# Kernel optimization log

Hardware: AMD Instinct MI355X
Metric: run time of the kernel (lower is better)

The kernel has to match this reference:

```python
import jax, jax.numpy as jnp
import numpy as np

V, D, H, B, S, K = 10000, 128, 512, 32, 512, 2  # vocab, emb, hidden, batch, seq, num_cells

def setup_inputs() -> dict:
    key = jax.random.key(0)
    ks = jax.random.split(key, 8)
    sc_d, sc_h = 1.0 / np.sqrt(D), 1.0 / np.sqrt(H)
    return {
        "x": jax.random.randint(ks[0], (B, S), 0, V),
        "emb_table": jax.random.normal(ks[1], (V, D), jnp.float32),
        "W_ih": jax.random.uniform(ks[2], (K, 4 * H, D), jnp.float32, -sc_d, sc_d),
        "W_hh": jax.random.uniform(ks[3], (K, 4 * H, H), jnp.float32, -sc_h, sc_h),
        "b_ih": jax.random.uniform(ks[4], (K, 4 * H), jnp.float32, -sc_h, sc_h),
        "b_hh": jax.random.uniform(ks[5], (K, 4 * H), jnp.float32, -sc_h, sc_h),
        "W_out": jax.random.uniform(ks[6], (V, H), jnp.float32, -sc_h, sc_h),
        "b_out": jax.random.uniform(ks[7], (V,), jnp.float32, -sc_h, sc_h),
    }

def _mlstm(x_ids_t, emb_t, W_ih, W_hh, b, h0, c0):
    # x_ids_t: (S,B) int, emb_t: (S,B,D). Two LSTMCells; token id parity picks the cell.
    def step(carry, inp):
        h, c = carry                       # (B,H) each
        xt, ids = inp                      # (B,D), (B,)
        gates = (jnp.einsum('bd,kgd->kbg', xt, W_ih)
                 + jnp.einsum('bh,kgh->kbg', h, W_hh)
                 + b[:, None, :])          # (K,B,4H)
        i, f, g, o = jnp.split(gates, 4, axis=-1)
        i, f, o = jax.nn.sigmoid(i), jax.nn.sigmoid(f), jax.nn.sigmoid(o)
        g = jnp.tanh(g)
        c_new = f * c + i * g              # (K,B,H)
        h_new = o * jnp.tanh(c_new)        # (K,B,H)
        sel = (ids % 2)[:, None]           # (B,1) cell index per example
        h_next = jnp.where(sel == 0, h_new[0], h_new[1])
        c_next = jnp.where(sel == 0, c_new[0], c_new[1])
        return (h_next, c_next), h_next
    (_, _), hs = jax.lax.scan(step, (h0, c0), (emb_t, x_ids_t))
    return hs  # (S,B,H)

def reference(x, emb_table, W_ih, W_hh, b_ih, b_hh, W_out, b_out):
    emb = emb_table[x]                     # (B,S,D)
    emb_t = jnp.transpose(emb, (1, 0, 2))  # (S,B,D) time-major
    h0 = jnp.zeros((x.shape[0], W_hh.shape[-1]), emb.dtype)
    hs = _mlstm(x.T, emb_t, W_ih, W_hh, b_ih + b_hh, h0, h0)  # (S,B,H)
    flat = hs.reshape(-1, hs.shape[-1])    # (S*B, H)
    logits = flat @ W_out.T + b_out        # (S*B, V)
    return jax.nn.log_softmax(logits, axis=1)
```

## Files before the change

### kernel.cpp

```cpp
#include <hip/hip_runtime.h>
#include <hip/hip_bf16.h>

typedef __attribute__((ext_vector_type(8))) short short8;
typedef __attribute__((ext_vector_type(4))) float f32x4;
typedef unsigned long long u64;

#define V_N 10000
#define D_E 128
#define H_N 512
#define B_N 32
#define S_N 512

#define SENT64 0xFFFFFFFFFFFFFFFFull

#define OFF_RP    0
#define OFF_EMB   5242880
#define OFF_HS    (OFF_EMB + 4194304)
#define OFF_WOUT  (OFF_HS + 16777216)

__device__ __forceinline__ float ftanh(float x) {
  float e = __expf(-2.f * fabsf(x));
  float r = (1.f - e) / (1.f + e);
  return __builtin_copysignf(r, x);
}

union U128 { f32x4 f; u64 q[2]; };

__global__ void k_prep_emb(const int* __restrict__ x, const float* __restrict__ tab,
                           __hip_bfloat16* __restrict__ emb) {
  int i = blockIdx.x * 256 + threadIdx.x;
  if (i >= S_N * B_N * D_E) return;
  int d  = i & (D_E - 1);
  int sb = i >> 7;
  int b  = sb & (B_N - 1);
  int s  = sb >> 5;
  int tok = x[b * S_N + s];
  emb[i] = __float2bfloat16(tab[tok * D_E + d]);
}

__global__ void k_prep_wout(const float* __restrict__ w, __hip_bfloat16* __restrict__ o) {
  int i = blockIdx.x * 256 + threadIdx.x;
  if (i < V_N * H_N) o[i] = __float2bfloat16(w[i]);
}

__launch_bounds__(512, 1)
__global__ void k_recurrence(const int* __restrict__ x,
                             const float* __restrict__ W_ih, const float* __restrict__ W_hh,
                             const float* __restrict__ b_ih, const float* __restrict__ b_hh,
                             const __hip_bfloat16* __restrict__ emb,
                             __hip_bfloat16* __restrict__ hs)
{
  __shared__ __align__(16) __hip_bfloat16 Bl[32][648];
  __shared__ float gl[128][34];
  __shared__ float bias[128];
  __shared__ unsigned short hloc[16][32];

  const int tid = threadIdx.x;
  const int wg  = blockIdx.x;
  const int lane = tid & 63, wv = tid >> 6;
  const int lrow = lane & 15, lk = (lane >> 4) * 8;
  const int b_ep = tid & 31, jj_ep = tid >> 5;

  short8 Afrag[20];
  #pragma unroll
  for (int ks = 0; ks < 20; ++ks) {
    int lr = wv * 16 + lrow;
    int q = lr >> 5, kc = (lr >> 4) & 1, jj = lr & 15;
    int grow = kc * 2048 + q * 512 + wg * 16 + jj;
    int c0 = ks * 32 + lk;
    short8 a;
    #pragma unroll
    for (int e = 0; e < 8; ++e) {
      int c = c0 + e;
      float v = (c < 128) ? W_ih[(size_t)grow * 128 + c]
                          : W_hh[(size_t)grow * 512 + (c - 128)];
      __hip_bfloat16 hb = __float2bfloat16(v);
      a[e] = *(const short*)&hb;
    }
    Afrag[ks] = a;
  }
  if (tid < 128) {
    int lr = tid;
    int q = lr >> 5, kc = (lr >> 4) & 1, jj = lr & 15;
    int grow = kc * 2048 + q * 512 + wg * 16 + jj;
    bias[lr] = b_ih[grow] + b_hh[grow];
  }

  unsigned par[16];
  #pragma unroll
  for (int w = 0; w < 16; ++w) {
    unsigned p = 0;
    for (int bb = 0; bb < 32; ++bb)
      p |= (unsigned)(x[b_ep * S_N + w * 32 + bb] & 1) << bb;
    par[w] = p;
  }

  float c_state = 0.f;

  for (int t = 0; t < S_N; ++t) {
    {
      const f32x4* e16 = (const f32x4*)(emb + (size_t)t * B_N * D_E);
      int ex = tid >> 4, col = tid & 15;
      *(f32x4*)((char*)&Bl[0][0] + ex * 1296 + col * 16) = e16[tid];
    }
    if (t == 0) {
      for (int i = tid; i < 4096; i += 512) {
        int b = i >> 7, hh = i & 127;
        *(u64*)&Bl[b][128 + hh * 4] = 0ull;
      }
    } else {
      const char* srcb = (const char*)hs + (size_t)(t - 1) * 32768;
      U128 buf[4];
      unsigned pend = 0xFu;
      while (pend) {
        #pragma unroll
        for (int c = 0; c < 4; ++c)
          if (pend & (1u << c))
            asm volatile("global_load_dwordx4 %0, %1, off sc0 sc1"
                         : "=v"(buf[c].f) : "v"(srcb + (c * 8192 + tid * 16)) : "memory");
        asm volatile("s_waitcnt vmcnt(0)" ::: "memory");
        __builtin_amdgcn_sched_barrier(0);
        #pragma unroll
        for (int c = 0; c < 4; ++c)
          if ((pend & (1u << c)) && buf[c].q[0] != SENT64 && buf[c].q[1] != SENT64) {
            int ci = c * 512 + tid;
            *(f32x4*)((char*)&Bl[0][0] + (ci >> 6) * 1296 + 256 + (ci & 63) * 16) = buf[c].f;
            pend &= ~(1u << c);
          }
      }
    }
    __syncthreads();

    {
      f32x4 acc0 = {0.f,0.f,0.f,0.f}, acc1 = {0.f,0.f,0.f,0.f};
      #pragma unroll
      for (int ks = 0; ks < 20; ++ks) {
        int cb = (ks * 32 + lk) * 2;
        short8 b0 = *(const short8*)((const char*)&Bl[0][0] + lrow * 1296 + cb);
        short8 b1 = *(const short8*)((const char*)&Bl[0][0] + (16 + lrow) * 1296 + cb);
        acc0 = __builtin_amdgcn_mfma_f32_16x16x32_bf16(Afrag[ks], b0, acc0, 0, 0, 0);
        acc1 = __builtin_amdgcn_mfma_f32_16x16x32_bf16(Afrag[ks], b1, acc1, 0, 0, 0);
      }
      int r0 = wv * 16 + (lane >> 4) * 4;
      int cb0 = lane & 15;
      #pragma unroll
      for (int r = 0; r < 4; ++r) {
        gl[r0 + r][cb0]      = acc0[r];
        gl[r0 + r][16 + cb0] = acc1[r];
      }
    }
    __syncthreads();

    {
      float cand_c[2], cand_h[2];
      #pragma unroll
      for (int kc = 0; kc < 2; ++kc) {
        int base = kc * 16 + jj_ep;
        float ig = gl[base][b_ep]      + bias[base];
        float fg = gl[32 + base][b_ep] + bias[32 + base];
        float gg = gl[64 + base][b_ep] + bias[64 + base];
        float og = gl[96 + base][b_ep] + bias[96 + base];
        ig = 1.f / (1.f + __expf(-ig));
        fg = 1.f / (1.f + __expf(-fg));
        og = 1.f / (1.f + __expf(-og));
        gg = ftanh(gg);
        float cn = fg * c_state + ig * gg;
        cand_c[kc] = cn;
        cand_h[kc] = og * ftanh(cn);
      }
      int sel = (par[t >> 5] >> (t & 31)) & 1;
      c_state  = sel ? cand_c[1] : cand_c[0];
      float hv = sel ? cand_h[1] : cand_h[0];
      __hip_bfloat16 hb = __float2bfloat16(hv);
      hloc[jj_ep][b_ep] = *(const unsigned short*)&hb;
    }
    __syncthreads();

    if (tid < 128) {
      int ex = tid >> 2, part = tid & 3;
      u64 v = (u64)hloc[part * 4 + 0][ex]
            | ((u64)hloc[part * 4 + 1][ex] << 16)
            | ((u64)hloc[part * 4 + 2][ex] << 32)
            | ((u64)hloc[part * 4 + 3][ex] << 48);
      u64* dst = (u64*)hs + (size_t)t * 4096 + ex * 128 + wg * 4 + part;
      __hip_atomic_store(dst, v, __ATOMIC_RELAXED, __HIP_MEMORY_SCOPE_AGENT);
    }
  }
}

__launch_bounds__(256, 2)
__global__ void k_gemm(const __hip_bfloat16* __restrict__ hs,
                       const __hip_bfloat16* __restrict__ wout,
                       const float* __restrict__ b_out,
                       float* __restrict__ out,
                       float* __restrict__ rowpart)
{
  __shared__ __hip_bfloat16 Al[128][72];
  __shared__ __hip_bfloat16 Wt[128][72];
  __shared__ float sumLDS[2][128];
  const int tid = threadIdx.x;
  const int tn = blockIdx.x, tm = blockIdx.y;
  const int lane = tid & 63, wv = tid >> 6;
  const int mq = wv & 1, nq = wv >> 1;
  const int lrow = lane & 15, lk = (lane >> 4) * 8;
  f32x4 acc[4][4] = {};

  const int ar = tid >> 3, ac = (tid & 7) * 8;
  for (int k0 = 0; k0 < 512; k0 += 64) {
    __syncthreads();
    #pragma unroll
    for (int rr = 0; rr < 4; ++rr) {
      int r = ar + rr * 32;
      short8 av = *(const short8*)(hs + ((size_t)(tm * 128 + r)) * 512 + k0 + ac);
      *(short8*)&Al[r][ac] = av;
      int v = tn * 128 + r;
      short8 wvv = {};
      if (v < V_N) wvv = *(const short8*)(wout + (size_t)v * 512 + k0 + ac);
      *(short8*)&Wt[r][ac] = wvv;
    }
    __syncthreads();
    #pragma unroll
    for (int ks = 0; ks < 2; ++ks) {
      int kb = ks * 32 + lk;
      short8 af[4], bf[4];
      #pragma unroll
      for (int i = 0; i < 4; ++i) af[i] = *(const short8*)&Al[mq * 64 + i * 16 + lrow][kb];
      #pragma unroll
      for (int i = 0; i < 4; ++i) bf[i] = *(const short8*)&Wt[nq * 64 + i * 16 + lrow][kb];
      #pragma unroll
      for (int i = 0; i < 4; ++i)
        #pragma unroll
        for (int jx = 0; jx < 4; ++jx)
          acc[i][jx] = __builtin_amdgcn_mfma_f32_16x16x32_bf16(af[i], bf[jx], acc[i][jx], 0, 0, 0);
    }
  }
  const int rbase = tm * 128 + mq * 64 + (lane >> 4) * 4;
  const int cbase = tn * 128 + nq * 64 + (lane & 15);
  float esum[4][4];
  #pragma unroll
  for (int i = 0; i < 4; ++i)
    #pragma unroll
    for (int r = 0; r < 4; ++r) esum[i][r] = 0.f;

  #pragma unroll
  for (int i = 0; i < 4; ++i) {
    #pragma unroll
    for (int jx = 0; jx < 4; ++jx) {
      int col = cbase + jx * 16;
      if (col < V_N) {
        float bo = b_out[col];
        #pragma unroll
        for (int r = 0; r < 4; ++r) {
          int row = rbase + i * 16 + r;
          float lg = acc[i][jx][r] + bo;
          out[(size_t)row * V_N + col] = lg;
          esum[i][r] += __expf(lg);
        }
      }
    }
  }
  #pragma unroll
  for (int i = 0; i < 4; ++i) {
    #pragma unroll
    for (int r = 0; r < 4; ++r) {
      float s = esum[i][r];
      s += __shfl_xor(s, 1); s += __shfl_xor(s, 2);
      s += __shfl_xor(s, 4); s += __shfl_xor(s, 8);
      if ((lane & 15) == 0)
        sumLDS[nq][mq * 64 + i * 16 + (lane >> 4) * 4 + r] = s;
    }
  }
  __syncthreads();
  if (tid < 128)
    rowpart[(size_t)(tm * 128 + tid) * 80 + tn] = sumLDS[0][tid] + sumLDS[1][tid];
}

__launch_bounds__(256)
__global__ void k_lsm_fix(float* __restrict__ out, const float* __restrict__ rowpart) {
  const int r = blockIdx.x;
  const float* rp = rowpart + (size_t)r * 80;
  float s = 0.f;
  for (int p = 0; p < 79; ++p) s += rp[p];
  float lse = __logf(s);
  float4* q4 = (float4*)(out + (size_t)r * V_N);
  for (int i = threadIdx.x; i < V_N / 4; i += 256) {
    float4 v = q4[i];
    v.x -= lse; v.y -= lse; v.z -= lse; v.w -= lse;
    q4[i] = v;
  }
}

extern "C" void kernel_launch(void* const* d_in, const int* in_sizes, int n_in,
                              void* d_out, int out_size, void* d_ws, size_t ws_size,
                              hipStream_t stream) {
  const int*   x    = (const int*)d_in[0];
  const float* tab  = (const float*)d_in[1];
  const float* Wih  = (const float*)d_in[2];
  const float* Whh  = (const float*)d_in[3];
  const float* bih  = (const float*)d_in[4];
  const float* bhh  = (const float*)d_in[5];
  const float* Wout = (const float*)d_in[6];
  const float* bout = (const float*)d_in[7];
  float* out = (float*)d_out;

  char* ws = (char*)d_ws;
  float*           rowpart = (float*)(ws + OFF_RP);
  __hip_bfloat16*  emb     = (__hip_bfloat16*)(ws + OFF_EMB);
  __hip_bfloat16*  hsbuf   = (__hip_bfloat16*)(ws + OFF_HS);
  __hip_bfloat16*  wob     = (__hip_bfloat16*)(ws + OFF_WOUT);

  hipMemsetAsync(hsbuf, 0xFF, (size_t)S_N * B_N * H_N * 2, stream);
  k_prep_emb<<<(S_N * B_N * D_E) / 256, 256, 0, stream>>>(x, tab, emb);
  k_prep_wout<<<(V_N * H_N) / 256, 256, 0, stream>>>(Wout, wob);
  k_recurrence<<<32, 512, 0, stream>>>(x, Wih, Whh, bih, bhh, emb, hsbuf);
  k_gemm<<<dim3(79, 128), 256, 0, stream>>>(hsbuf, wob, bout, out, rowpart);
  k_lsm_fix<<<16384, 256, 0, stream>>>(out, rowpart);
}
```

Baseline: 2.456 ms.

## Stage logits as bf16 in output buffer and pipeline hidden-state polling loads

Result: slower. 2.707 ms (+10.2%).

```diff
diff --git a/kernel.cpp b/kernel.cpp
--- a/kernel.cpp
+++ b/kernel.cpp
@@ -111,23 +111,35 @@
     } else {
       const char* srcb = (const char*)hs + (size_t)(t - 1) * 32768;
       U128 buf[4];
+#define ISSUE(c) asm volatile("global_load_dwordx4 %0, %1, off sc0 sc1" \
+        : "=v"(buf[c].f) : "v"(srcb + ((c) * 8192 + tid * 16)) : "memory")
+#define WAITN(n) do { int _n = (n); \
+        if (_n == 0)      asm volatile("s_waitcnt vmcnt(0)" ::: "memory"); \
+        else if (_n == 1) asm volatile("s_waitcnt vmcnt(1)" ::: "memory"); \
+        else              asm volatile("s_waitcnt vmcnt(2)" ::: "memory"); \
+        __builtin_amdgcn_sched_barrier(0); } while (0)
+#define CHK(c, bit) if ((pend & (bit)) && buf[c].q[0] != SENT64 && buf[c].q[1] != SENT64) { \
+        int ci = (c) * 512 + tid; \
+        *(f32x4*)((char*)&Bl[0][0] + (ci >> 6) * 1296 + 256 + (ci & 63) * 16) = buf[c].f; \
+        pend &= ~(unsigned)(bit); }
       unsigned pend = 0xFu;
+      int nA = 2, nB = 2;
+      ISSUE(0); ISSUE(1); ISSUE(2); ISSUE(3);
       while (pend) {
-        #pragma unroll
-        for (int c = 0; c < 4; ++c)
-          if (pend & (1u << c))
-            asm volatile("global_load_dwordx4 %0, %1, off sc0 sc1"
-                         : "=v"(buf[c].f) : "v"(srcb + (c * 8192 + tid * 16)) : "memory");
-        asm volatile("s_waitcnt vmcnt(0)" ::: "memory");
-        __builtin_amdgcn_sched_barrier(0);
-        #pragma unroll
-        for (int c = 0; c < 4; ++c)
-          if ((pend & (1u << c)) && buf[c].q[0] != SENT64 && buf[c].q[1] != SENT64) {
-            int ci = c * 512 + tid;
-            *(f32x4*)((char*)&Bl[0][0] + (ci >> 6) * 1296 + 256 + (ci & 63) * 16) = buf[c].f;
-            pend &= ~(1u << c);
-          }
-      }
+        WAITN(nB);
+        CHK(0, 1u) CHK(1, 2u)
+        nA = 0;
+        if (pend & 1u) { ISSUE(0); ++nA; }
+        if (pend & 2u) { ISSUE(1); ++nA; }
+        WAITN(nA);
+        CHK(2, 4u) CHK(3, 8u)
+        nB = 0;
+        if (pend & 4u) { ISSUE(2); ++nB; }
+        if (pend & 8u) { ISSUE(3); ++nB; }
+      }
+#undef ISSUE
+#undef WAITN
+#undef CHK
     }
     __syncthreads();
 
@@ -253,7 +265,9 @@
         for (int r = 0; r < 4; ++r) {
           int row = rbase + i * 16 + r;
           float lg = acc[i][jx][r] + bo;
-          out[(size_t)row * V_N + col] = lg;
+          __hip_bfloat16* lrow16 =
+            (__hip_bfloat16*)((char*)out + (size_t)row * (V_N * 4) + V_N * 2);
+          lrow16[col] = __float2bfloat16(lg);
           esum[i][r] += __expf(lg);
         }
       }
@@ -278,15 +292,38 @@
 __launch_bounds__(256)
 __global__ void k_lsm_fix(float* __restrict__ out, const float* __restrict__ rowpart) {
   const int r = blockIdx.x;
+  const int tid = threadIdx.x;
   const float* rp = rowpart + (size_t)r * 80;
   float s = 0.f;
   for (int p = 0; p < 79; ++p) s += rp[p];
   float lse = __logf(s);
-  float4* q4 = (float4*)(out + (size_t)r * V_N);
-  for (int i = threadIdx.x; i < V_N / 4; i += 256) {
-    float4 v = q4[i];
-    v.x -= lse; v.y -= lse; v.z -= lse; v.w -= lse;
-    q4[i] = v;
+
+  const f32x4* src = (const f32x4*)((const char*)out + (size_t)r * (V_N * 4) + V_N * 2);
+  U128 c[5];
+  #pragma unroll
+  for (int i = 0; i < 5; ++i) {
+    int idx = tid + i * 256;
+    if (idx < 1250) c[i].f = src[idx];
+  }
+  __syncthreads();
+  float* dst = out + (size_t)r * V_N;
+  #pragma unroll
+  for (int i = 0; i < 5; ++i) {
+    int idx = tid + i * 256;
+    if (idx < 1250) {
+      const unsigned short* u = (const unsigned short*)&c[i];
+      float4 lo, hi;
+      lo.x = __uint_as_float((unsigned)u[0] << 16) - lse;
+      lo.y = __uint_as_float((unsigned)u[1] << 16) - lse;
+      lo.z = __uint_as_float((unsigned)u[2] << 16) - lse;
+      lo.w = __uint_as_float((unsigned)u[3] << 16) - lse;
+      hi.x = __uint_as_float((unsigned)u[4] << 16) - lse;
+      hi.y = __uint_as_float((unsigned)u[5] << 16) - lse;
+      hi.z = __uint_as_float((unsigned)u[6] << 16) - lse;
+      hi.w = __uint_as_float((unsigned)u[7] << 16) - lse;
+      *(float4*)(dst + idx * 8)     = lo;
+      *(float4*)(dst + idx * 8 + 4) = hi;
+    }
   }
 }
 
```
